# Kernel optimization log

Hardware: AMD Instinct MI355X
Metric: run time of the kernel (lower is better)

## Reference

```python
import jax, jax.numpy as jnp
import numpy as np

N = 1024      # layer_size (power of 2)
B = 16384     # batch
DEPTH = 2     # Butterfly depth (default)


def _abcd_offsets(n):
    """Factor sizes n, n/2, ..., 2 and their offsets into the packed ABCD buffer.
    A factor of size m has ABCD of shape (2, 2, m//2, 2) = 2m complex pairs."""
    offs = []
    off = 0
    m = n
    while m >= 2:
        offs.append((m, off))
        off += 2 * m
        m //= 2
    return offs, off  # off == 4n - 4


def setup_inputs() -> dict:
    key = jax.random.key(0)
    k1, k2, k3 = jax.random.split(key, 3)
    _, total = _abcd_offsets(N)
    x = jax.random.normal(k1, (B, N), jnp.float32)
    perm_logit = jax.random.normal(k2, (DEPTH, 3), jnp.float32)
    # scale ~1/sqrt(2) so the product of log2(n) random 2x2 blocks stays bounded
    abcd = jax.random.normal(k3, (DEPTH, total, 2), jnp.float32) * 0.7
    b = jnp.zeros((N,), jnp.float32)
    return {"x": x, "perm_logit": perm_logit, "abcd": abcd, "b": b}


def _perm_factor(h, p, m):
    """One BlockPerm factor (soft permutation) of size m applied blockwise.
    h: (B, n, 2) real/imag pairs. p: (3,) probabilities.
    p[0]: mix with even/odd separation; p[1], p[2]: mix each half with its reversal."""
    Bn, n, _ = h.shape
    h = h.reshape(Bn, n // m, m, 2)
    eo = jnp.concatenate([h[:, :, 0::2], h[:, :, 1::2]], axis=2)
    h = (1 - p[0]) * h + p[0] * eo
    h1, h2 = h[:, :, : m // 2], h[:, :, m // 2 :]
    h1 = (1 - p[1]) * h1 + p[1] * h1[:, :, ::-1]
    h2 = (1 - p[2]) * h2 + p[2] * h2[:, :, ::-1]
    return jnp.concatenate([h1, h2], axis=2).reshape(Bn, n, 2)


def _diag_factor(h, ABCD, m):
    """One Block2x2Diag factor of size m: out = [[A,B],[C,D]] x with diagonal A,B,C,D.
    h: (B, n, 2); ABCD: (2, 2, m//2, 2) complex pairs."""
    Bn, n, _ = h.shape
    hv = h.reshape(Bn, n // m, 2, m // 2, 2)  # (B, blocks, halves, m/2, cplx)
    xr, xi = hv[..., 0], hv[..., 1]
    Ar, Ai = ABCD[..., 0], ABCD[..., 1]
    yr = jnp.einsum('ijk,bnjk->bnik', Ar, xr) - jnp.einsum('ijk,bnjk->bnik', Ai, xi)
    yi = jnp.einsum('ijk,bnjk->bnik', Ar, xi) + jnp.einsum('ijk,bnjk->bnik', Ai, xr)
    return jnp.stack([yr, yi], axis=-1).reshape(Bn, n, 2)


def _forward(x, perm_logit, abcd, b):
    n = x.shape[-1]
    offs, _ = _abcd_offsets(n)
    # real_to_complex: (B, n) -> (B, n, 2)
    h = jnp.stack([x, jnp.zeros_like(x)], axis=-1)
    perm_sizes = [m for (m, _) in offs if m >= 4]
    depth = perm_logit.shape[0]
    for d in range(depth):
        # BlockPermProduct (share_logit=True): all factors share one (3,) logit
        p = jax.nn.sigmoid(perm_logit[d])
        for m in reversed(perm_sizes):      # smallest factor first
            h = _perm_factor(h, p, m)
        # Block2x2DiagProduct: factors applied smallest size first
        for (m, off) in reversed(offs):
            ABCD = abcd[d, off:off + 2 * m].reshape(2, 2, m // 2, 2)
            h = _diag_factor(h, ABCD, m)
    out = h[..., 0]  # take real part
    return b + out


def reference(x, perm_logit, abcd, b):
    return _forward(x, perm_logit, abcd, b)
```

## Files before the change

### kernel.cpp

```cpp
#include <hip/hip_runtime.h>
#include <hip/hip_bf16.h>
#include <stdint.h>

#define N_DIM 1024
#define DEPTH 2
#define ABCD_TOTAL 4092

typedef __attribute__((ext_vector_type(8))) short short8;
typedef __attribute__((ext_vector_type(4))) float floatx4;
typedef __attribute__((ext_vector_type(4))) float f4;

__device__ __forceinline__ f4 cmul(float cr, float ci, f4 v) {
    f4 r;
    r[0] = cr * v[0] - ci * v[1];
    r[1] = cr * v[1] + ci * v[0];
    r[2] = cr * v[2] - ci * v[3];
    r[3] = cr * v[3] + ci * v[2];
    return r;
}

__global__ __launch_bounds__(256) void build_and_cast(
    const float* __restrict__ perm_logit,
    const float* __restrict__ abcd,
    const float* __restrict__ x,
    __hip_bfloat16* __restrict__ S,
    __hip_bfloat16* __restrict__ xb)
{
    const int bx  = blockIdx.x;
    const int tid = threadIdx.x;
    __shared__ f4 h[2][N_DIM];

    if (bx >= 512) {
        const int cb = bx - 512;
        const size_t i = ((size_t)cb * 256 + tid) * 8;
        float4 v0 = *(const float4*)(x + i);
        float4 v1 = *(const float4*)(x + i + 4);
        union { __hip_bfloat16 e[8]; int4 v; } u;
        u.e[0] = __float2bfloat16(v0.x); u.e[1] = __float2bfloat16(v0.y);
        u.e[2] = __float2bfloat16(v0.z); u.e[3] = __float2bfloat16(v0.w);
        u.e[4] = __float2bfloat16(v1.x); u.e[5] = __float2bfloat16(v1.y);
        u.e[6] = __float2bfloat16(v1.z); u.e[7] = __float2bfloat16(v1.w);
        *(int4*)(xb + i) = u.v;
        return;
    }

    const int row0 = bx * 2;
    const f4 zz = {0.0f, 0.0f, 0.0f, 0.0f};
    for (int j = tid; j < N_DIM; j += 256) { h[0][j] = zz; h[1][j] = zz; }
    __syncthreads();
    if (tid == 0) {
        f4 e0 = {1.0f, 0.0f, 0.0f, 0.0f};
        f4 e1 = {0.0f, 0.0f, 1.0f, 0.0f};
        h[0][row0]     = e0;
        h[0][row0 + 1] = e1;
    }
    __syncthreads();

    int cur = 0;
    for (int d = 0; d < DEPTH; ++d) {
        const float p0 = 1.0f / (1.0f + expf(-perm_logit[d * 3 + 0]));
        const float p1 = 1.0f / (1.0f + expf(-perm_logit[d * 3 + 1]));
        const float p2 = 1.0f / (1.0f + expf(-perm_logit[d * 3 + 2]));

#pragma unroll
        for (int s = 2; s <= 10; ++s) {
            if (s >= 8) __syncthreads();
            else        __builtin_amdgcn_wave_barrier();
            const int half = 1 << (s - 1), hq = half >> 1;
            const int cnt   = (d == 0) ? half : 512;
            const int pbase = (d == 0) ? ((row0 >> s) << (s - 1)) : 0;
            const f4* __restrict__ in = h[cur];
            f4* __restrict__ out      = h[cur ^ 1];
            for (int tt = tid; tt < cnt; tt += 256) {
                const int t    = pbase + tt;
                const int blk  = t >> (s - 1);
                const int r    = t & (half - 1);
                const int base = blk << s;
                int q1, q2; float pc;
                if (r < hq) { q1 = r;           q2 = half - 1 - r;   pc = p1; }
                else        { int r2 = r - hq;  q1 = half + r2;
                              q2 = 2 * half - 1 - r2;                pc = p2; }
                const int src1 = (q1 < half) ? 2 * q1 : 2 * (q1 - half) + 1;
                const int src2 = (q2 < half) ? 2 * q2 : 2 * (q2 - half) + 1;
                f4 b1 = in[base + q1], a1 = in[base + src1];
                f4 b2 = in[base + q2], a2 = in[base + src2];
                f4 s1a = b1 + p0 * (a1 - b1);
                f4 s1b = b2 + p0 * (a2 - b2);
                out[base + q1] = s1a + pc * (s1b - s1a);
                out[base + q2] = s1b + pc * (s1a - s1b);
            }
            cur ^= 1;
        }
        __syncthreads();

        const float* __restrict__ abd = abcd + (size_t)d * (ABCD_TOTAL * 2);
#pragma unroll
        for (int s = 1; s <= 9; s += 2) {
            if (s == 9) __syncthreads();
            else        __builtin_amdgcn_wave_barrier();
            const int hh = 1 << (s - 1);
            const float* __restrict__ ab1 = abd + (size_t)(4096 - 8 * hh) * 2;
            const float* __restrict__ ab2 = abd + (size_t)(4096 - 16 * hh) * 2;
            const f4* __restrict__ in = h[cur];
            f4* __restrict__ out      = h[cur ^ 1];
            {
                const int g     = tid;
                const int k     = g & (hh - 1);
                const int base2 = (g >> (s - 1)) << (s + 1);
                f4 x0 = in[base2 + k];
                f4 x1 = in[base2 + k + hh];
                f4 x2 = in[base2 + k + 2 * hh];
                f4 x3 = in[base2 + k + 3 * hh];
                float2 A = *(const float2*)(ab1 + 2 * (size_t)k);
                float2 B = *(const float2*)(ab1 + 2 * (size_t)(hh + k));
                float2 C = *(const float2*)(ab1 + 2 * (size_t)(2 * hh + k));
                float2 D = *(const float2*)(ab1 + 2 * (size_t)(3 * hh + k));
                f4 y0 = cmul(A.x, A.y, x0) + cmul(B.x, B.y, x1);
                f4 y1 = cmul(C.x, C.y, x0) + cmul(D.x, D.y, x1);
                f4 y2 = cmul(A.x, A.y, x2) + cmul(B.x, B.y, x3);
                f4 y3 = cmul(C.x, C.y, x2) + cmul(D.x, D.y, x3);
                float2 A2 = *(const float2*)(ab2 + 2 * (size_t)k);
                float2 B2 = *(const float2*)(ab2 + 2 * (size_t)(2 * hh + k));
                float2 C2 = *(const float2*)(ab2 + 2 * (size_t)(4 * hh + k));
                float2 D2 = *(const float2*)(ab2 + 2 * (size_t)(6 * hh + k));
                float2 A3 = *(const float2*)(ab2 + 2 * (size_t)(hh + k));
                float2 B3 = *(const float2*)(ab2 + 2 * (size_t)(3 * hh + k));
                float2 C3 = *(const float2*)(ab2 + 2 * (size_t)(5 * hh + k));
                float2 D3 = *(const float2*)(ab2 + 2 * (size_t)(7 * hh + k));
                out[base2 + k]          = cmul(A2.x, A2.y, y0) + cmul(B2.x, B2.y, y2);
                out[base2 + k + 2 * hh] = cmul(C2.x, C2.y, y0) + cmul(D2.x, D2.y, y2);
                out[base2 + k + hh]     = cmul(A3.x, A3.y, y1) + cmul(B3.x, B3.y, y3);
                out[base2 + k + 3 * hh] = cmul(C3.x, C3.y, y1) + cmul(D3.x, D3.y, y3);
            }
            cur ^= 1;
        }
        __syncthreads();
    }

    for (int j = tid; j < N_DIM; j += 256) {
        f4 v = h[cur][j];
        S[(size_t)row0 * N_DIM + j]       = __float2bfloat16(v[0]);
        S[(size_t)(row0 + 1) * N_DIM + j] = __float2bfloat16(v[2]);
    }
}

__global__ __launch_bounds__(256) void transpose_w(
    const __hip_bfloat16* __restrict__ S, __hip_bfloat16* __restrict__ Wt)
{
    const int i0 = (blockIdx.x & 15) * 64;
    const int j0 = (blockIdx.x >> 4) * 64;
    __shared__ __hip_bfloat16 tile[64][72];
    const int r  = threadIdx.x >> 2;
    const int c0 = (threadIdx.x & 3) * 16;
    *(short8*)&tile[r][c0]     = *(const short8*)(S + (size_t)(i0 + r) * N_DIM + j0 + c0);
    *(short8*)&tile[r][c0 + 8] = *(const short8*)(S + (size_t)(i0 + r) * N_DIM + j0 + c0 + 8);
    __syncthreads();
    union { __hip_bfloat16 e[8]; short8 v; } o1, o2;
#pragma unroll
    for (int k = 0; k < 8; ++k) { o1.e[k] = tile[c0 + k][r]; o2.e[k] = tile[c0 + 8 + k][r]; }
    *(short8*)(Wt + (size_t)(j0 + r) * N_DIM + i0 + c0)     = o1.v;
    *(short8*)(Wt + (size_t)(j0 + r) * N_DIM + i0 + c0 + 8) = o2.v;
}

#define BM 128
#define BN 128
#define BK 64

__device__ __forceinline__ void gl_lds16(const void* g, void* l) {
    __builtin_amdgcn_global_load_lds(
        (const __attribute__((address_space(1))) uint32_t*)g,
        (__attribute__((address_space(3))) uint32_t*)l, 16, 0, 0);
}

__global__ __launch_bounds__(256, 4) void gemm_bt(
    const __hip_bfloat16* __restrict__ A,
    const __hip_bfloat16* __restrict__ Bt,
    const float* __restrict__ bias,
    float* __restrict__ C)
{
    const int tid = threadIdx.x;
    const int bx  = blockIdx.x;
    const int xcd = bx & 7;
    const int loc = bx >> 3;
    const int m0  = (xcd * 16 + (loc >> 3)) * BM;
    const int n0  = (loc & 7) * BN;

    __shared__ __hip_bfloat16 sA[BM * BK];
    __shared__ __hip_bfloat16 sB[BN * BK];

    const int lane = tid & 63;
    const int wm   = ((tid >> 6) & 1) * 64;
    const int wn   = ((tid >> 6) >> 1) * 64;
    const int lrow = lane & 15;
    const int lq   = lane >> 4;

    const int r1 = tid >> 3;
    const int cs = (tid & 7) ^ (r1 & 7);
    const int swz = lrow & 7;

    floatx4 acc[4][4] = {};

    for (int kt = 0; kt < 16; ++kt) {
        const int k0 = kt * BK;
#pragma unroll
        for (int i = 0; i < 4; ++i)
            gl_lds16(A + (size_t)(m0 + r1 + i * 32) * N_DIM + k0 + cs * 8,
                     (char*)sA + (tid + i * 256) * 16);
#pragma unroll
        for (int i = 0; i < 4; ++i)
            gl_lds16(Bt + (size_t)(n0 + r1 + i * 32) * N_DIM + k0 + cs * 8,
                     (char*)sB + (tid + i * 256) * 16);
        __syncthreads();

#pragma unroll
        for (int ks = 0; ks < 2; ++ks) {
            short8 af[4], bf[4];
            const int cc = (lq + 4 * ks) ^ swz;
#pragma unroll
            for (int i = 0; i < 4; ++i) {
                af[i] = *(const short8*)((const char*)sA + (((wm + i * 16 + lrow) * 8 + cc) * 16));
                bf[i] = *(const short8*)((const char*)sB + (((wn + i * 16 + lrow) * 8 + cc) * 16));
            }
#pragma unroll
            for (int i = 0; i < 4; ++i)
#pragma unroll
                for (int j = 0; j < 4; ++j)
                    acc[i][j] = __builtin_amdgcn_mfma_f32_16x16x32_bf16(
                        bf[j], af[i], acc[i][j], 0, 0, 0);
        }
        __syncthreads();
    }

#pragma unroll
    for (int i = 0; i < 4; ++i) {
        const int gm = m0 + wm + i * 16 + lrow;
#pragma unroll
        for (int j = 0; j < 4; ++j) {
            const int gn = n0 + wn + j * 16 + lq * 4;
            const float4 bv = *(const float4*)(bias + gn);
            floatx4 a = acc[i][j];
            float4 o;
            o.x = a[0] + bv.x; o.y = a[1] + bv.y;
            o.z = a[2] + bv.z; o.w = a[3] + bv.w;
            *(float4*)(C + (size_t)gm * N_DIM + gn) = o;
        }
    }
}

extern "C" void kernel_launch(void* const* d_in, const int* in_sizes, int n_in,
                              void* d_out, int out_size, void* d_ws, size_t ws_size,
                              hipStream_t stream) {
    const float* x          = (const float*)d_in[0];
    const float* perm_logit = (const float*)d_in[1];
    const float* abcd       = (const float*)d_in[2];
    const float* bias       = (const float*)d_in[3];
    float* out              = (float*)d_out;

    __hip_bfloat16* S  = (__hip_bfloat16*)d_out;
    __hip_bfloat16* Wt = (__hip_bfloat16*)d_ws;
    __hip_bfloat16* xb = (__hip_bfloat16*)((char*)d_ws + (1 << 21));

    build_and_cast<<<dim3(512 + 8192), dim3(256), 0, stream>>>(perm_logit, abcd, x, S, xb);
    transpose_w<<<dim3(256), dim3(256), 0, stream>>>(S, Wt);
    gemm_bt<<<dim3(1024), dim3(256), 0, stream>>>(xb, Wt, bias, out);
}
```

Before: 158.3 us.

## Fuse fp32-to-bf16 cast of x into GEMM A-tile loads

```diff
diff --git a/kernel.cpp b/kernel.cpp
--- a/kernel.cpp
+++ b/kernel.cpp
@@ -19,30 +19,14 @@
     return r;
 }
 
-__global__ __launch_bounds__(256) void build_and_cast(
+__global__ __launch_bounds__(256) void build_w(
     const float* __restrict__ perm_logit,
     const float* __restrict__ abcd,
-    const float* __restrict__ x,
-    __hip_bfloat16* __restrict__ S,
-    __hip_bfloat16* __restrict__ xb)
+    __hip_bfloat16* __restrict__ S)
 {
     const int bx  = blockIdx.x;
     const int tid = threadIdx.x;
     __shared__ f4 h[2][N_DIM];
-
-    if (bx >= 512) {
-        const int cb = bx - 512;
-        const size_t i = ((size_t)cb * 256 + tid) * 8;
-        float4 v0 = *(const float4*)(x + i);
-        float4 v1 = *(const float4*)(x + i + 4);
-        union { __hip_bfloat16 e[8]; int4 v; } u;
-        u.e[0] = __float2bfloat16(v0.x); u.e[1] = __float2bfloat16(v0.y);
-        u.e[2] = __float2bfloat16(v0.z); u.e[3] = __float2bfloat16(v0.w);
-        u.e[4] = __float2bfloat16(v1.x); u.e[5] = __float2bfloat16(v1.y);
-        u.e[6] = __float2bfloat16(v1.z); u.e[7] = __float2bfloat16(v1.w);
-        *(int4*)(xb + i) = u.v;
-        return;
-    }
 
     const int row0 = bx * 2;
     const f4 zz = {0.0f, 0.0f, 0.0f, 0.0f};
@@ -172,8 +156,8 @@
         (__attribute__((address_space(3))) uint32_t*)l, 16, 0, 0);
 }
 
-__global__ __launch_bounds__(256, 4) void gemm_bt(
-    const __hip_bfloat16* __restrict__ A,
+__global__ __launch_bounds__(256, 3) void gemm_xf32(
+    const float* __restrict__ X,
     const __hip_bfloat16* __restrict__ Bt,
     const float* __restrict__ bias,
     float* __restrict__ C)
@@ -185,8 +169,8 @@
     const int m0  = (xcd * 16 + (loc >> 3)) * BM;
     const int n0  = (loc & 7) * BN;
 
-    __shared__ __hip_bfloat16 sA[BM * BK];
-    __shared__ __hip_bfloat16 sB[BN * BK];
+    __shared__ __attribute__((aligned(128))) char smem[49152];
+    char* const sB = smem + 32768;
 
     const int lane = tid & 63;
     const int wm   = ((tid >> 6) & 1) * 64;
@@ -203,23 +187,36 @@
     for (int kt = 0; kt < 16; ++kt) {
         const int k0 = kt * BK;
 #pragma unroll
-        for (int i = 0; i < 4; ++i)
-            gl_lds16(A + (size_t)(m0 + r1 + i * 32) * N_DIM + k0 + cs * 8,
-                     (char*)sA + (tid + i * 256) * 16);
+        for (int i = 0; i < 8; ++i) {
+            const int h = i >> 2;
+            const int r = r1 + (i & 3) * 32;
+            gl_lds16(X + (size_t)(m0 + r) * N_DIM + k0 + h * 32 + cs * 4,
+                     smem + (tid + i * 256) * 16);
+        }
 #pragma unroll
         for (int i = 0; i < 4; ++i)
             gl_lds16(Bt + (size_t)(n0 + r1 + i * 32) * N_DIM + k0 + cs * 8,
-                     (char*)sB + (tid + i * 256) * 16);
+                     sB + (tid + i * 256) * 16);
         __syncthreads();
 
 #pragma unroll
         for (int ks = 0; ks < 2; ++ks) {
             short8 af[4], bf[4];
             const int cc = (lq + 4 * ks) ^ swz;
+            const int c0p = (2 * lq) ^ swz;
+            const int c1p = (2 * lq + 1) ^ swz;
 #pragma unroll
             for (int i = 0; i < 4; ++i) {
-                af[i] = *(const short8*)((const char*)sA + (((wm + i * 16 + lrow) * 8 + cc) * 16));
-                bf[i] = *(const short8*)((const char*)sB + (((wn + i * 16 + lrow) * 8 + cc) * 16));
+                const char* rowp = smem + ks * 16384 + (wm + i * 16 + lrow) * 128;
+                float4 v0 = *(const float4*)(rowp + c0p * 16);
+                float4 v1 = *(const float4*)(rowp + c1p * 16);
+                union { __hip_bfloat16 e[8]; short8 v; } ua;
+                ua.e[0] = __float2bfloat16(v0.x); ua.e[1] = __float2bfloat16(v0.y);
+                ua.e[2] = __float2bfloat16(v0.z); ua.e[3] = __float2bfloat16(v0.w);
+                ua.e[4] = __float2bfloat16(v1.x); ua.e[5] = __float2bfloat16(v1.y);
+                ua.e[6] = __float2bfloat16(v1.z); ua.e[7] = __float2bfloat16(v1.w);
+                af[i] = ua.v;
+                bf[i] = *(const short8*)(sB + (((wn + i * 16 + lrow) * 8 + cc) * 16));
             }
 #pragma unroll
             for (int i = 0; i < 4; ++i)
@@ -258,9 +255,8 @@
 
     __hip_bfloat16* S  = (__hip_bfloat16*)d_out;
     __hip_bfloat16* Wt = (__hip_bfloat16*)d_ws;
-    __hip_bfloat16* xb = (__hip_bfloat16*)((char*)d_ws + (1 << 21));
-
-    build_and_cast<<<dim3(512 + 8192), dim3(256), 0, stream>>>(perm_logit, abcd, x, S, xb);
+
+    build_w<<<dim3(512), dim3(256), 0, stream>>>(perm_logit, abcd, S);
     transpose_w<<<dim3(256), dim3(256), 0, stream>>>(S, Wt);
-    gemm_bt<<<dim3(1024), dim3(256), 0, stream>>>(xb, Wt, bias, out);
-}
+    gemm_xf32<<<dim3(1024), dim3(256), 0, stream>>>(x, Wt, bias, out);
+}
```

Result: slower. 191.2 us (+20.8%).
